# Performance work log

Measured on AMD Instinct MI355X. Metric: run time of the kernel, lower is better.

The kernel has to match this reference:

```python
import jax, jax.numpy as jnp
import numpy as np

EMBED_DIM = 1024
NUM_HEADS = 16
HEAD_DIM = EMBED_DIM // NUM_HEADS
B, N = 2, 2048
BIAS_S = 32


def _interp_matrix(n, s):
    # Bilinear interpolation (align_corners=True) along one axis as an (n, s) matrix.
    pos = jnp.arange(n, dtype=jnp.float32) * ((s - 1) / (n - 1))
    i0 = jnp.floor(pos).astype(jnp.int32)
    i1 = jnp.minimum(i0 + 1, s - 1)
    frac = pos - i0.astype(jnp.float32)
    rows = jnp.arange(n)
    M = jnp.zeros((n, s), dtype=jnp.float32)
    M = M.at[rows, i0].add(1.0 - frac).at[rows, i1].add(frac)
    return M


def setup_inputs() -> dict:
    key = jax.random.key(0)
    ks = jax.random.split(key, 12)
    std = 0.02
    d = {
        'x': jax.random.normal(ks[0], (B, N, EMBED_DIM), dtype=jnp.float32),
        'Wq': jax.random.normal(ks[1], (EMBED_DIM, EMBED_DIM), dtype=jnp.float32) * std,
        'bq': jnp.zeros((EMBED_DIM,), dtype=jnp.float32),
        'Wk': jax.random.normal(ks[2], (EMBED_DIM, EMBED_DIM), dtype=jnp.float32) * std,
        'bk': jnp.zeros((EMBED_DIM,), dtype=jnp.float32),
        'Wv': jax.random.normal(ks[3], (EMBED_DIM, EMBED_DIM), dtype=jnp.float32) * std,
        'bv': jnp.zeros((EMBED_DIM,), dtype=jnp.float32),
        'Wo': jax.random.normal(ks[4], (EMBED_DIM, EMBED_DIM), dtype=jnp.float32) * std,
        'bo': jnp.zeros((EMBED_DIM,), dtype=jnp.float32),
        'gamma': jnp.ones((EMBED_DIM,), dtype=jnp.float32),
        'beta': jnp.zeros((EMBED_DIM,), dtype=jnp.float32),
        'rel_bias': jax.random.normal(ks[5], (NUM_HEADS, BIAS_S, BIAS_S), dtype=jnp.float32) * std,
    }
    return d


def reference(x, Wq, bq, Wk, bk, Wv, bv, Wo, bo, gamma, beta, rel_bias):
    Bx, Nx, C = x.shape
    H, D = NUM_HEADS, HEAD_DIM
    scale = 1.0 / jnp.sqrt(jnp.float32(D))

    # LayerNorm
    mu = jnp.mean(x, axis=-1, keepdims=True)
    var = jnp.mean(jnp.square(x - mu), axis=-1, keepdims=True)
    xn = (x - mu) * jax.lax.rsqrt(var + 1e-5) * gamma + beta

    q = (xn @ Wq.T + bq).reshape(Bx, Nx, H, D).transpose(0, 2, 1, 3)
    k = (xn @ Wk.T + bk).reshape(Bx, Nx, H, D).transpose(0, 2, 1, 3)
    v = (xn @ Wv.T + bv).reshape(Bx, Nx, H, D).transpose(0, 2, 1, 3)

    attn = jnp.einsum('bhnd,bhmd->bhnm', q, k) * scale  # [B,H,N,N]

    # Bilinear interp of rel_pos_bias (H,32,32) -> (H,N,N), align_corners=True
    M = _interp_matrix(Nx, BIAS_S)  # (N, 32)
    rel = jnp.einsum('ni,hij,mj->hnm', M, rel_bias, M)
    rel = rel.at[:, -1, :].set(0.0).at[:, :, -1].set(0.0)
    attn = attn + rel[None]

    mask = jnp.triu(jnp.ones((Nx, Nx), dtype=bool), k=1)
    attn = jnp.where(mask, -jnp.inf, attn)
    attn = jax.nn.softmax(attn, axis=-1)

    out = jnp.einsum('bhnm,bhmd->bhnd', attn, v)
    out = out.transpose(0, 2, 1, 3).reshape(Bx, Nx, C)
    out = out @ Wo.T + bo  # dropout is identity in eval mode
    return out
```

## Files before the change

### kernel.cpp

```cpp
#include <hip/hip_runtime.h>
#include <hip/hip_bf16.h>

#define EMBED 1024
#define NHEADS 16
#define HDIM 64
#define NB 2
#define NSEQ 2048
#define NTOK (NB*NSEQ)

using short8  = __attribute__((ext_vector_type(8))) short;
using short4v = __attribute__((ext_vector_type(4))) short;
using f32x4   = __attribute__((ext_vector_type(4))) float;

#define INV_LN2 1.4426950408889634f

__device__ __forceinline__ short f2bf(float x) {
  __hip_bfloat16 h = __float2bfloat16(x);
  short s;
  __builtin_memcpy(&s, &h, 2);
  return s;
}

#define GLDS16(gp, lp) __builtin_amdgcn_global_load_lds( \
    (const __attribute__((address_space(1))) unsigned int*)(const void*)(gp), \
    (__attribute__((address_space(3))) unsigned int*)(void*)(lp), 16, 0, 0)

__global__ __launch_bounds__(256) void lncast_kernel(const float* __restrict__ x,
    const float* __restrict__ gamma, const float* __restrict__ beta, short* __restrict__ xn,
    const float* __restrict__ Wq, const float* __restrict__ Wk,
    const float* __restrict__ Wv, const float* __restrict__ Wo,
    short* __restrict__ wqb, short* __restrict__ wkb,
    short* __restrict__ wvb, short* __restrict__ wob) {
  const int bid = blockIdx.x;
  const int tid = threadIdx.x;
  if (bid < NTOK) {
    const float* xr = x + (size_t)bid * EMBED;
    float4 v = *(const float4*)(xr + tid * 4);
    float s  = v.x + v.y + v.z + v.w;
    float s2 = v.x*v.x + v.y*v.y + v.z*v.z + v.w*v.w;
#pragma unroll
    for (int off = 32; off; off >>= 1) {
      s  += __shfl_down(s, off);
      s2 += __shfl_down(s2, off);
    }
    __shared__ float red[8];
    const int wv = tid >> 6, ln = tid & 63;
    if (ln == 0) { red[wv] = s; red[4 + wv] = s2; }
    __syncthreads();
    s  = red[0] + red[1] + red[2] + red[3];
    s2 = red[4] + red[5] + red[6] + red[7];
    const float mu  = s * (1.0f / EMBED);
    const float var = s2 * (1.0f / EMBED) - mu * mu;
    const float inv = rsqrtf(var + 1e-5f);
    float4 g  = *(const float4*)(gamma + tid * 4);
    float4 bt = *(const float4*)(beta + tid * 4);
    short4v o;
    o[0] = f2bf((v.x - mu) * inv * g.x + bt.x);
    o[1] = f2bf((v.y - mu) * inv * g.y + bt.y);
    o[2] = f2bf((v.z - mu) * inv * g.z + bt.z);
    o[3] = f2bf((v.w - mu) * inv * g.w + bt.w);
    *(short4v*)(xn + (size_t)bid * EMBED + tid * 4) = o;
  } else {
    const int i = (bid - NTOK) * 1024 + tid * 4;
    const int wsel = i >> 20;
    const int off  = i & 1048575;
    const float* s = (wsel == 0) ? Wq : (wsel == 1) ? Wk : (wsel == 2) ? Wv : Wo;
    short* o       = (wsel == 0) ? wqb : (wsel == 1) ? wkb : (wsel == 2) ? wvb : wob;
    float4 v = *(const float4*)(s + off);
    short4v r;
    r[0] = f2bf(v.x); r[1] = f2bf(v.y); r[2] = f2bf(v.z); r[3] = f2bf(v.w);
    *(short4v*)(o + off) = r;
  }
}

__global__ __launch_bounds__(512, 4) void qkv2ph_kernel(
    const short* __restrict__ A, const short* __restrict__ Wcat,
    const float* __restrict__ b0, const float* __restrict__ b1, const float* __restrict__ b2,
    short* __restrict__ O0, short* __restrict__ O1, short* __restrict__ O2) {
  constexpr int K = 1024;
  const int orig = blockIdx.x;
  const int swzb = (orig & 7) * 64 + (orig >> 3);
  const int tn = swzb & 15, tm = swzb >> 4;

  const int tid = threadIdx.x;
  const int w = tid >> 6, lane = tid & 63;
  const int wr = w >> 2, wc = w & 3;
  const int g = lane >> 4, c = lane & 15;

  __shared__ short As[2][128 * 64];
  __shared__ short Bs[2][192 * 64];

  f32x4 acc[4][3];
#pragma unroll
  for (int i = 0; i < 4; i++)
#pragma unroll
    for (int j = 0; j < 3; j++) acc[i][j] = (f32x4){0.f, 0.f, 0.f, 0.f};

  const int sr  = tid >> 3;
  const int sc8 = (tid & 7) * 8;
  const int ssw = (sr & 7) << 3;
  const short* ga = A    + (size_t)(tm * 128) * K;
  const short* gb = Wcat + (size_t)(tn * 192) * K;

  auto STAGE = [&](int buf, int kt) {
#pragma unroll
    for (int u = 0; u < 2; u++) {
      const int row = u * 64 + sr;
      GLDS16(ga + (size_t)row * K + kt * 64 + (sc8 ^ ssw), &As[buf][row * 64 + sc8]);
    }
#pragma unroll
    for (int u = 0; u < 3; u++) {
      const int row = u * 64 + sr;
      GLDS16(gb + (size_t)row * K + kt * 64 + (sc8 ^ ssw), &Bs[buf][row * 64 + sc8]);
    }
  };

  STAGE(0, 0);
  __syncthreads();

  for (int kt = 0; kt < 16; ++kt) {
    const int cur = kt & 1;
    if (kt + 1 < 16) STAGE(cur ^ 1, kt + 1);
    const short* as = As[cur];
    const short* bs = Bs[cur];
#pragma unroll
    for (int ks = 0; ks < 2; ks++) {
      short8 af[4], bf[3];
#pragma unroll
      for (int mi = 0; mi < 4; mi++) {
        const int row = wr * 64 + mi * 16 + c;
        af[mi] = *(const short8*)&as[row * 64 + ((ks * 32 + g * 8) ^ ((row & 7) << 3))];
      }
#pragma unroll
      for (int ni = 0; ni < 3; ni++) {
        const int row = wc * 48 + ni * 16 + c;
        bf[ni] = *(const short8*)&bs[row * 64 + ((ks * 32 + g * 8) ^ ((row & 7) << 3))];
      }
      __builtin_amdgcn_s_setprio(1);
#pragma unroll
      for (int mi = 0; mi < 4; mi++)
#pragma unroll
        for (int ni = 0; ni < 3; ni++)
          acc[mi][ni] = __builtin_amdgcn_mfma_f32_16x16x32_bf16(af[mi], bf[ni], acc[mi][ni], 0, 0, 0);
      __builtin_amdgcn_s_setprio(0);
    }
    __syncthreads();
  }

#pragma unroll
  for (int ni = 0; ni < 3; ni++) {
    const int col = tn * 192 + wc * 48 + ni * 16 + c;
    const int sel = col >> 10, lc = col & 1023;
    short* O        = (sel == 0) ? O0 : (sel == 1) ? O1 : O2;
    const float* bb = (sel == 0) ? b0 : (sel == 1) ? b1 : b2;
    const float bsv = bb[lc];
#pragma unroll
    for (int mi = 0; mi < 4; mi++) {
      const int row = tm * 128 + wr * 64 + mi * 16 + g * 4;
#pragma unroll
      for (int j = 0; j < 4; j++)
        O[(size_t)(row + j) * 1024 + lc] = f2bf(acc[mi][ni][j] + bsv);
    }
  }
}

template<bool F32OUT>
__global__ __launch_bounds__(256) void gemm_kernel(
    const short* __restrict__ A, const short* __restrict__ Bw,
    const float* __restrict__ bias, void* __restrict__ Cout) {
  constexpr int K = 1024, NOUT = 1024;
  const int tn = blockIdx.x, tm = blockIdx.y;
  const int tid = threadIdx.x, w = tid >> 6, lane = tid & 63;
  const int wm = w >> 1, wn = w & 1;
  const int g = lane >> 4, c = lane & 15;

  __shared__ short As[128 * 32];
  __shared__ short Bs[128 * 32];

  f32x4 acc[4][4];
#pragma unroll
  for (int i = 0; i < 4; i++)
#pragma unroll
    for (int j = 0; j < 4; j++) acc[i][j] = (f32x4){0.f, 0.f, 0.f, 0.f};

  const int crow = tid >> 2;
  const int ckc  = tid & 3;
  const short* ga = A  + (size_t)(tm * 128 + crow) * K + ckc * 8;
  const short* gb = Bw + (size_t)(tn * 128 + crow) * K + ckc * 8;
  short* la = &As[tid * 8];
  short* lb = &Bs[tid * 8];

  for (int k0 = 0; k0 < K; k0 += 32) {
    __syncthreads();
    GLDS16(ga + k0, la);
    GLDS16(ga + k0 + (size_t)64 * K, la + 64 * 32);
    GLDS16(gb + k0, lb);
    GLDS16(gb + k0 + (size_t)64 * K, lb + 64 * 32);
    __syncthreads();
    short8 af[4], bfr[4];
#pragma unroll
    for (int mi = 0; mi < 4; mi++)
      af[mi] = *(const short8*)&As[(wm * 64 + mi * 16 + c) * 32 + g * 8];
#pragma unroll
    for (int ni = 0; ni < 4; ni++)
      bfr[ni] = *(const short8*)&Bs[(wn * 64 + ni * 16 + c) * 32 + g * 8];
#pragma unroll
    for (int mi = 0; mi < 4; mi++)
#pragma unroll
      for (int ni = 0; ni < 4; ni++)
        acc[mi][ni] = __builtin_amdgcn_mfma_f32_16x16x32_bf16(af[mi], bfr[ni], acc[mi][ni], 0, 0, 0);
  }

#pragma unroll
  for (int ni = 0; ni < 4; ni++) {
    const int col = tn * 128 + wn * 64 + ni * 16 + c;
    const float bs = bias[col];
#pragma unroll
    for (int mi = 0; mi < 4; mi++) {
#pragma unroll
      for (int j = 0; j < 4; j++) {
        const int row = tm * 128 + wm * 64 + mi * 16 + g * 4 + j;
        const float v = acc[mi][ni][j] + bs;
        if constexpr (F32OUT)
          ((float*)Cout)[(size_t)row * NOUT + col] = v;
        else
          ((short*)Cout)[(size_t)row * NOUT + col] = f2bf(v);
      }
    }
  }
}

__global__ __launch_bounds__(256) void vtrans_kernel(const short* __restrict__ vb,
                                                     short* __restrict__ vt) {
  const int n0 = blockIdx.x * 64;
  const int bh = blockIdx.y;
  const int b = bh >> 4, h = bh & 15;
  const int tid = threadIdx.x;
  __shared__ short tl[64 * 68];

  const int r  = tid >> 3;
  const int c8 = (tid & 7) * 8;
#pragma unroll
  for (int i = 0; i < 2; i++) {
    const int row = r + i * 32;
    short8 v = *(const short8*)(vb + (size_t)(b * NSEQ + n0 + row) * EMBED + h * 64 + c8);
    *(short8*)&tl[row * 68 + c8] = v;
  }
  __syncthreads();
  const int d  = tid >> 2;
  const int ns = (tid & 3) * 16;
  short8 o0, o1;
#pragma unroll
  for (int e = 0; e < 8; e++) {
    o0[e] = tl[(ns + e) * 68 + d];
    o1[e] = tl[(ns + 8 + e) * 68 + d];
  }
  short* dst = vt + ((size_t)((b * 16 + h) * 64 + d)) * 2048 + n0 + ns;
  *(short8*)dst = o0;
  *(short8*)(dst + 8) = o1;
}

__global__ __launch_bounds__(512, 4) void attn_kernel(
    const short* __restrict__ Qm, const short* __restrict__ Km, const short* __restrict__ Vt,
    const float* __restrict__ relb, short* __restrict__ ctx) {
  const int bid = blockIdx.x;
  const int bh  = bid & 31;
  const int idx = bid >> 5;
  const int qpair = (idx < 8) ? (15 - idx) : (idx - 8);
  const int b = bh >> 4, h = bh & 15;
  const int tid = threadIdx.x, w = tid >> 6, lane = tid & 63;
  const int g = lane >> 4, c = lane & 15;
  constexpr float S31 = 31.0f / 2047.0f;
  constexpr float CSC = 0.125f * INV_LN2;

  __shared__ short k_lds[2][64 * 64];
  __shared__ short vt_lds[2][64 * 64];
  __shared__ short p_lds[8][16 * 64];
  __shared__ short rbf[128 * 32];
  __shared__ short u_lds[2][64 * 40];

  const int qbase = qpair * 128;
  const size_t bhq = (size_t)b * NSEQ * EMBED + h * HDIM;
  const short* vtb = Vt + (size_t)((b << 4) + h) * 64 * 2048;

  short8 qf[2];
  {
    const short* qp = Qm + bhq + (size_t)(qbase + w * 16 + c) * EMBED;
    qf[0] = *(const short8*)(qp + g * 8);
    qf[1] = *(const short8*)(qp + 32 + g * 8);
  }

  const int srow = tid >> 3;
  const int sd0  = (tid & 7) * 8;
  const int swz  = (srow & 7) << 3;

  auto buildU = [&](int buf, int kv) {
    if (tid < 64) {
      short* ur = &u_lds[buf][tid * 40];
      *(int4*)&ur[0]  = (int4){0, 0, 0, 0};
      *(int4*)&ur[8]  = (int4){0, 0, 0, 0};
      *(int4*)&ur[16] = (int4){0, 0, 0, 0};
      *(int4*)&ur[24] = (int4){0, 0, 0, 0};
      const int m = kv + tid;
      if (m != NSEQ - 1) {
        const float pos = m * S31;
        const int i0 = (int)pos;
        const float fr = pos - (float)i0;
        ur[i0]     = f2bf(1.0f - fr);
        ur[i0 + 1] = f2bf(fr);
      }
    }
  };

  GLDS16(Km + bhq + (size_t)srow * EMBED + (sd0 ^ swz), &k_lds[0][srow * 64 + sd0]);
  GLDS16(vtb + (size_t)srow * 2048 + (sd0 ^ swz),       &vt_lds[0][srow * 64 + sd0]);
  for (int i = tid; i < 128 * 32; i += 512) {
    const int qr = i >> 5, jj = i & 31;
    const int qg0 = qbase + qr;
    float rv = 0.f;
    if (qg0 != NSEQ - 1) {
      const float pos = qg0 * S31;
      const int i0 = (int)pos;
      const int i1 = min(i0 + 1, 31);
      const float fr = pos - (float)i0;
      const float* T = relb + h * 1024;
      rv = ((1.f - fr) * T[i0 * 32 + jj] + fr * T[i1 * 32 + jj]) * 8.0f;
    }
    rbf[i] = f2bf(rv);
  }
  buildU(0, 0);
  __syncthreads();

  const short8 rq = *(const short8*)&rbf[(w * 16 + c) * 32 + g * 8];

  float mrow = -3.0e38f, lrow = 0.f;
  f32x4 oacc[4];
#pragma unroll
  for (int db = 0; db < 4; db++) oacc[db] = (f32x4){0.f, 0.f, 0.f, 0.f};

  const int qg  = qbase + w * 16 + c;
  const int qhi = qbase + w * 16 + 15;
  const int csw = (c & 7) << 3;
  const int nkv = 2 * qpair + 2;

  for (int kt = 0; kt < nkv; kt++) {
    const int cur = kt & 1;
    const int kv0 = kt * 64;

    if (kt + 1 < nkv) {
      GLDS16(Km + bhq + (size_t)(kv0 + 64 + srow) * EMBED + (sd0 ^ swz),
             &k_lds[cur ^ 1][srow * 64 + sd0]);
      GLDS16(vtb + (size_t)srow * 2048 + (kv0 + 64) + (sd0 ^ swz),
             &vt_lds[cur ^ 1][srow * 64 + sd0]);
      buildU(cur ^ 1, kv0 + 64);
    }

    if (kv0 <= qhi) {
      const short* kl = &k_lds[cur][0];
      const short* vl = &vt_lds[cur][0];
      const short* ul = &u_lds[cur][0];

      f32x4 st[4];
#pragma unroll
      for (int mb = 0; mb < 4; mb++) st[mb] = (f32x4){0.f, 0.f, 0.f, 0.f};
      __builtin_amdgcn_s_setprio(1);
#pragma unroll
      for (int kh = 0; kh < 2; kh++) {
        const int dk = kh * 32 + g * 8;
#pragma unroll
        for (int mb = 0; mb < 4; mb++) {
          const int row = mb * 16 + c;
          short8 kf = *(const short8*)&kl[row * 64 + (dk ^ ((row & 7) << 3))];
          st[mb] = __builtin_amdgcn_mfma_f32_16x16x32_bf16(kf, qf[kh], st[mb], 0, 0, 0);
        }
      }
#pragma unroll
      for (int mb = 0; mb < 4; mb++) {
        short8 uf = *(const short8*)&ul[(mb * 16 + c) * 40 + g * 8];
        st[mb] = __builtin_amdgcn_mfma_f32_16x16x32_bf16(uf, rq, st[mb], 0, 0, 0);
      }
      __builtin_amdgcn_s_setprio(0);

      const bool diag = (kv0 + 63 > qg);
      if (diag) {
#pragma unroll
        for (int mb = 0; mb < 4; mb++)
#pragma unroll
          for (int j = 0; j < 4; j++) {
            const int mg = kv0 + mb * 16 + g * 4 + j;
            if (mg > qg) st[mb][j] = -1.0e38f;
          }
      }
      float pmr = -3.0e38f;
#pragma unroll
      for (int mb = 0; mb < 4; mb++)
#pragma unroll
        for (int j = 0; j < 4; j++) pmr = fmaxf(pmr, st[mb][j]);
      float pmax = pmr * CSC;
      pmax = fmaxf(pmax, __shfl_xor(pmax, 16));
      pmax = fmaxf(pmax, __shfl_xor(pmax, 32));

      if (!__all(pmax - mrow <= 11.6f)) {
        const float mnew = fmaxf(mrow, pmax);
        const float al = exp2f(mrow - mnew);
        mrow = mnew;
        lrow *= al;
        float alj[4];
#pragma unroll
        for (int j = 0; j < 4; j++) alj[j] = __shfl(al, g * 4 + j);
#pragma unroll
        for (int db = 0; db < 4; db++)
#pragma unroll
          for (int j = 0; j < 4; j++) oacc[db][j] *= alj[j];
      }

      float p[4][4];
      float rs = 0.f;
#pragma unroll
      for (int mb = 0; mb < 4; mb++)
#pragma unroll
        for (int j = 0; j < 4; j++) {
          const float pe = exp2f(fmaf(st[mb][j], CSC, -mrow));
          p[mb][j] = pe;
          rs += pe;
        }
      rs += __shfl_xor(rs, 16);
      rs += __shfl_xor(rs, 32);
      lrow += rs;

      short* pw = &p_lds[w][0];
#pragma unroll
      for (int mb = 0; mb < 4; mb++)
#pragma unroll
        for (int jh = 0; jh < 2; jh++) {
          const int m = mb * 16 + g * 4 + jh * 2;
          unsigned int pk = ((unsigned int)(unsigned short)f2bf(p[mb][jh * 2 + 1]) << 16)
                          |  (unsigned int)(unsigned short)f2bf(p[mb][jh * 2]);
          *(unsigned int*)&pw[c * 64 + (m ^ csw)] = pk;
        }

      __builtin_amdgcn_s_setprio(1);
#pragma unroll
      for (int kb = 0; kb < 2; kb++) {
        const int m0 = kb * 32 + g * 8;
        short8 pa = *(const short8*)&pw[c * 64 + (m0 ^ csw)];
#pragma unroll
        for (int db = 0; db < 4; db++) {
          const int d = db * 16 + c;
          short8 vf = *(const short8*)&vl[d * 64 + (m0 ^ ((d & 7) << 3))];
          oacc[db] = __builtin_amdgcn_mfma_f32_16x16x32_bf16(pa, vf, oacc[db], 0, 0, 0);
        }
      }
      __builtin_amdgcn_s_setprio(0);
    }
    __syncthreads();
  }

  float linv[4];
#pragma unroll
  for (int j = 0; j < 4; j++) linv[j] = 1.f / __shfl(lrow, g * 4 + j);
#pragma unroll
  for (int j = 0; j < 4; j++) {
    short* op = ctx + bhq + (size_t)(qbase + w * 16 + g * 4 + j) * EMBED;
#pragma unroll
    for (int db = 0; db < 4; db++)
      op[db * 16 + c] = f2bf(oacc[db][j] * linv[j]);
  }
}

extern "C" void kernel_launch(void* const* d_in, const int* in_sizes, int n_in,
                              void* d_out, int out_size, void* d_ws, size_t ws_size,
                              hipStream_t stream) {
  const float* x     = (const float*)d_in[0];
  const float* Wq    = (const float*)d_in[1];
  const float* bq    = (const float*)d_in[2];
  const float* Wk    = (const float*)d_in[3];
  const float* bk    = (const float*)d_in[4];
  const float* Wv    = (const float*)d_in[5];
  const float* bv    = (const float*)d_in[6];
  const float* Wo    = (const float*)d_in[7];
  const float* bo    = (const float*)d_in[8];
  const float* gamma = (const float*)d_in[9];
  const float* beta  = (const float*)d_in[10];
  const float* relb  = (const float*)d_in[11];
  float* out = (float*)d_out;

  char* ws = (char*)d_ws;
  short* xn  = (short*)ws; ws += (size_t)NTOK * EMBED * 2;
  short* wqb = (short*)ws; ws += (size_t)EMBED * EMBED * 2;
  short* wkb = (short*)ws; ws += (size_t)EMBED * EMBED * 2;
  short* wvb = (short*)ws; ws += (size_t)EMBED * EMBED * 2;
  short* wob = (short*)ws; ws += (size_t)EMBED * EMBED * 2;
  short* qb  = (short*)ws; ws += (size_t)NTOK * EMBED * 2;
  short* kb_ = (short*)ws; ws += (size_t)NTOK * EMBED * 2;
  short* vb  = (short*)ws; ws += (size_t)NTOK * EMBED * 2;
  short* ctx = (short*)ws; ws += (size_t)NTOK * EMBED * 2;
  short* vtb = xn;

  lncast_kernel<<<dim3(NTOK + 4096), dim3(256), 0, stream>>>(
      x, gamma, beta, xn, Wq, Wk, Wv, Wo, wqb, wkb, wvb, wob);
  qkv2ph_kernel<<<dim3(512), dim3(512), 0, stream>>>(
      xn, wqb, bq, bk, bv, qb, kb_, vb);
  vtrans_kernel<<<dim3(32, 32), dim3(256), 0, stream>>>(vb, vtb);
  attn_kernel<<<dim3(512), dim3(512), 0, stream>>>(qb, kb_, vtb, relb, ctx);
  gemm_kernel<true><<<dim3(8, 32), dim3(256), 0, stream>>>(ctx, wob, bo, (void*)out);
}
```

Measured before the change: 211.5 us.

## Give each attention wave 32 query rows and double-buffer the output projection

The attention kernel drops from 512 to 256 threads, and each wave now handles two 16-row query groups. This lets every K and V fragment read from LDS feed two MFMAs, halving LDS traffic per flop, at the cost of more registers and fewer waves to hide latency. The output-projection GEMM is replaced by a double-buffered 128x64 tile kernel with K-step 64, swizzled LDS, block-index swizzling for cache locality and a launch grid of 512 blocks. The aim is better load/compute overlap and more blocks in flight.

```diff
diff --git a/kernel.cpp b/kernel.cpp
--- a/kernel.cpp
+++ b/kernel.cpp
@@ -164,68 +164,90 @@
   }
 }
 
-template<bool F32OUT>
-__global__ __launch_bounds__(256) void gemm_kernel(
+__global__ __launch_bounds__(256, 2) void proj2ph_kernel(
     const short* __restrict__ A, const short* __restrict__ Bw,
-    const float* __restrict__ bias, void* __restrict__ Cout) {
-  constexpr int K = 1024, NOUT = 1024;
-  const int tn = blockIdx.x, tm = blockIdx.y;
-  const int tid = threadIdx.x, w = tid >> 6, lane = tid & 63;
-  const int wm = w >> 1, wn = w & 1;
+    const float* __restrict__ bias, float* __restrict__ Cout) {
+  constexpr int K = 1024;
+  const int orig = blockIdx.x;
+  const int swzb = (orig & 7) * 64 + (orig >> 3);
+  const int tn = swzb & 15, tm = swzb >> 4;
+
+  const int tid = threadIdx.x;
+  const int w = tid >> 6, lane = tid & 63;
+  const int wr = w >> 1, wc = w & 1;
   const int g = lane >> 4, c = lane & 15;
 
-  __shared__ short As[128 * 32];
-  __shared__ short Bs[128 * 32];
-
-  f32x4 acc[4][4];
+  __shared__ short As[2][128 * 64];
+  __shared__ short Bs[2][64 * 64];
+
+  f32x4 acc[4][2];
 #pragma unroll
   for (int i = 0; i < 4; i++)
 #pragma unroll
-    for (int j = 0; j < 4; j++) acc[i][j] = (f32x4){0.f, 0.f, 0.f, 0.f};
-
-  const int crow = tid >> 2;
-  const int ckc  = tid & 3;
-  const short* ga = A  + (size_t)(tm * 128 + crow) * K + ckc * 8;
-  const short* gb = Bw + (size_t)(tn * 128 + crow) * K + ckc * 8;
-  short* la = &As[tid * 8];
-  short* lb = &Bs[tid * 8];
-
-  for (int k0 = 0; k0 < K; k0 += 32) {
+    for (int j = 0; j < 2; j++) acc[i][j] = (f32x4){0.f, 0.f, 0.f, 0.f};
+
+  const int sr8 = tid >> 3;
+  const int sd0 = (tid & 7) * 8;
+  const short* ga = A  + (size_t)(tm * 128) * K;
+  const short* gb = Bw + (size_t)(tn * 64) * K;
+
+  auto STAGE = [&](int buf, int kt) {
+#pragma unroll
+    for (int i = 0; i < 4; i++) {
+      const int row = i * 32 + sr8;
+      const int sw = (row & 7) << 3;
+      GLDS16(ga + (size_t)row * K + kt * 64 + (sd0 ^ sw), &As[buf][row * 64 + sd0]);
+    }
+#pragma unroll
+    for (int i = 0; i < 2; i++) {
+      const int row = i * 32 + sr8;
+      const int sw = (row & 7) << 3;
+      GLDS16(gb + (size_t)row * K + kt * 64 + (sd0 ^ sw), &Bs[buf][row * 64 + sd0]);
+    }
+  };
+
+  STAGE(0, 0);
+  __syncthreads();
+
+  for (int kt = 0; kt < 16; ++kt) {
+    const int cur = kt & 1;
+    if (kt + 1 < 16) STAGE(cur ^ 1, kt + 1);
+    const short* as = As[cur];
+    const short* bs = Bs[cur];
+#pragma unroll
+    for (int ks = 0; ks < 2; ks++) {
+      short8 af[4], bf[2];
+#pragma unroll
+      for (int mi = 0; mi < 4; mi++) {
+        const int row = wr * 64 + mi * 16 + c;
+        af[mi] = *(const short8*)&as[row * 64 + ((ks * 32 + g * 8) ^ ((row & 7) << 3))];
+      }
+#pragma unroll
+      for (int ni = 0; ni < 2; ni++) {
+        const int row = wc * 32 + ni * 16 + c;
+        bf[ni] = *(const short8*)&bs[row * 64 + ((ks * 32 + g * 8) ^ ((row & 7) << 3))];
+      }
+      __builtin_amdgcn_s_setprio(1);
+#pragma unroll
+      for (int mi = 0; mi < 4; mi++)
+#pragma unroll
+        for (int ni = 0; ni < 2; ni++)
+          acc[mi][ni] = __builtin_amdgcn_mfma_f32_16x16x32_bf16(af[mi], bf[ni], acc[mi][ni], 0, 0, 0);
+      __builtin_amdgcn_s_setprio(0);
+    }
     __syncthreads();
-    GLDS16(ga + k0, la);
-    GLDS16(ga + k0 + (size_t)64 * K, la + 64 * 32);
-    GLDS16(gb + k0, lb);
-    GLDS16(gb + k0 + (size_t)64 * K, lb + 64 * 32);
-    __syncthreads();
-    short8 af[4], bfr[4];
-#pragma unroll
-    for (int mi = 0; mi < 4; mi++)
-      af[mi] = *(const short8*)&As[(wm * 64 + mi * 16 + c) * 32 + g * 8];
-#pragma unroll
-    for (int ni = 0; ni < 4; ni++)
-      bfr[ni] = *(const short8*)&Bs[(wn * 64 + ni * 16 + c) * 32 + g * 8];
-#pragma unroll
-    for (int mi = 0; mi < 4; mi++)
-#pragma unroll
-      for (int ni = 0; ni < 4; ni++)
-        acc[mi][ni] = __builtin_amdgcn_mfma_f32_16x16x32_bf16(af[mi], bfr[ni], acc[mi][ni], 0, 0, 0);
-  }
-
-#pragma unroll
-  for (int ni = 0; ni < 4; ni++) {
-    const int col = tn * 128 + wn * 64 + ni * 16 + c;
-    const float bs = bias[col];
+  }
+
+#pragma unroll
+  for (int ni = 0; ni < 2; ni++) {
+    const int col = tn * 64 + wc * 32 + ni * 16 + c;
+    const float bsv = bias[col];
 #pragma unroll
     for (int mi = 0; mi < 4; mi++) {
-#pragma unroll
-      for (int j = 0; j < 4; j++) {
-        const int row = tm * 128 + wm * 64 + mi * 16 + g * 4 + j;
-        const float v = acc[mi][ni][j] + bs;
-        if constexpr (F32OUT)
-          ((float*)Cout)[(size_t)row * NOUT + col] = v;
-        else
-          ((short*)Cout)[(size_t)row * NOUT + col] = f2bf(v);
-      }
+      const int row = tm * 128 + wr * 64 + mi * 16 + g * 4;
+#pragma unroll
+      for (int j = 0; j < 4; j++)
+        Cout[(size_t)(row + j) * 1024 + col] = acc[mi][ni][j] + bsv;
     }
   }
 }
@@ -260,7 +282,7 @@
   *(short8*)(dst + 8) = o1;
 }
 
-__global__ __launch_bounds__(512, 4) void attn_kernel(
+__global__ __launch_bounds__(256, 2) void attn_kernel(
     const short* __restrict__ Qm, const short* __restrict__ Km, const short* __restrict__ Vt,
     const float* __restrict__ relb, short* __restrict__ ctx) {
   const int bid = blockIdx.x;
@@ -275,7 +297,7 @@
 
   __shared__ short k_lds[2][64 * 64];
   __shared__ short vt_lds[2][64 * 64];
-  __shared__ short p_lds[8][16 * 64];
+  __shared__ short p_lds[4][32 * 64];
   __shared__ short rbf[128 * 32];
   __shared__ short u_lds[2][64 * 40];
 
@@ -283,16 +305,16 @@
   const size_t bhq = (size_t)b * NSEQ * EMBED + h * HDIM;
   const short* vtb = Vt + (size_t)((b << 4) + h) * 64 * 2048;
 
-  short8 qf[2];
-  {
-    const short* qp = Qm + bhq + (size_t)(qbase + w * 16 + c) * EMBED;
-    qf[0] = *(const short8*)(qp + g * 8);
-    qf[1] = *(const short8*)(qp + 32 + g * 8);
-  }
-
-  const int srow = tid >> 3;
-  const int sd0  = (tid & 7) * 8;
-  const int swz  = (srow & 7) << 3;
+  short8 qf[2][2];
+#pragma unroll
+  for (int grp = 0; grp < 2; grp++) {
+    const short* qp = Qm + bhq + (size_t)(qbase + w * 32 + grp * 16 + c) * EMBED;
+    qf[grp][0] = *(const short8*)(qp + g * 8);
+    qf[grp][1] = *(const short8*)(qp + 32 + g * 8);
+  }
+
+  const int sr8 = tid >> 3;
+  const int sd0 = (tid & 7) * 8;
 
   auto buildU = [&](int buf, int kv) {
     if (tid < 64) {
@@ -312,9 +334,14 @@
     }
   };
 
-  GLDS16(Km + bhq + (size_t)srow * EMBED + (sd0 ^ swz), &k_lds[0][srow * 64 + sd0]);
-  GLDS16(vtb + (size_t)srow * 2048 + (sd0 ^ swz),       &vt_lds[0][srow * 64 + sd0]);
-  for (int i = tid; i < 128 * 32; i += 512) {
+#pragma unroll
+  for (int i = 0; i < 2; i++) {
+    const int row = i * 32 + sr8;
+    const int sw = (row & 7) << 3;
+    GLDS16(Km + bhq + (size_t)row * EMBED + (sd0 ^ sw), &k_lds[0][row * 64 + sd0]);
+    GLDS16(vtb + (size_t)row * 2048 + (sd0 ^ sw),       &vt_lds[0][row * 64 + sd0]);
+  }
+  for (int i = tid; i < 128 * 32; i += 256) {
     const int qr = i >> 5, jj = i & 31;
     const int qg0 = qbase + qr;
     float rv = 0.f;
@@ -331,15 +358,20 @@
   buildU(0, 0);
   __syncthreads();
 
-  const short8 rq = *(const short8*)&rbf[(w * 16 + c) * 32 + g * 8];
-
-  float mrow = -3.0e38f, lrow = 0.f;
-  f32x4 oacc[4];
-#pragma unroll
-  for (int db = 0; db < 4; db++) oacc[db] = (f32x4){0.f, 0.f, 0.f, 0.f};
-
-  const int qg  = qbase + w * 16 + c;
-  const int qhi = qbase + w * 16 + 15;
+  short8 rq[2];
+#pragma unroll
+  for (int grp = 0; grp < 2; grp++)
+    rq[grp] = *(const short8*)&rbf[(w * 32 + grp * 16 + c) * 32 + g * 8];
+
+  float mrow[2] = {-3.0e38f, -3.0e38f}, lrow[2] = {0.f, 0.f};
+  f32x4 oacc[2][4];
+#pragma unroll
+  for (int grp = 0; grp < 2; grp++)
+#pragma unroll
+    for (int db = 0; db < 4; db++) oacc[grp][db] = (f32x4){0.f, 0.f, 0.f, 0.f};
+
+  const int qgg[2] = {qbase + w * 32 + c, qbase + w * 32 + 16 + c};
+  const int qhi = qbase + w * 32 + 31;
   const int csw = (c & 7) << 3;
   const int nkv = 2 * qpair + 2;
 
@@ -348,10 +380,15 @@
     const int kv0 = kt * 64;
 
     if (kt + 1 < nkv) {
-      GLDS16(Km + bhq + (size_t)(kv0 + 64 + srow) * EMBED + (sd0 ^ swz),
-             &k_lds[cur ^ 1][srow * 64 + sd0]);
-      GLDS16(vtb + (size_t)srow * 2048 + (kv0 + 64) + (sd0 ^ swz),
-             &vt_lds[cur ^ 1][srow * 64 + sd0]);
+#pragma unroll
+      for (int i = 0; i < 2; i++) {
+        const int row = i * 32 + sr8;
+        const int sw = (row & 7) << 3;
+        GLDS16(Km + bhq + (size_t)(kv0 + 64 + row) * EMBED + (sd0 ^ sw),
+               &k_lds[cur ^ 1][row * 64 + sd0]);
+        GLDS16(vtb + (size_t)row * 2048 + (kv0 + 64) + (sd0 ^ sw),
+               &vt_lds[cur ^ 1][row * 64 + sd0]);
+      }
       buildU(cur ^ 1, kv0 + 64);
     }
 
@@ -360,9 +397,12 @@
       const short* vl = &vt_lds[cur][0];
       const short* ul = &u_lds[cur][0];
 
-      f32x4 st[4];
-#pragma unroll
-      for (int mb = 0; mb < 4; mb++) st[mb] = (f32x4){0.f, 0.f, 0.f, 0.f};
+      f32x4 st[2][4];
+#pragma unroll
+      for (int grp = 0; grp < 2; grp++)
+#pragma unroll
+        for (int mb = 0; mb < 4; mb++) st[grp][mb] = (f32x4){0.f, 0.f, 0.f, 0.f};
+
       __builtin_amdgcn_s_setprio(1);
 #pragma unroll
       for (int kh = 0; kh < 2; kh++) {
@@ -371,84 +411,101 @@
         for (int mb = 0; mb < 4; mb++) {
           const int row = mb * 16 + c;
           short8 kf = *(const short8*)&kl[row * 64 + (dk ^ ((row & 7) << 3))];
-          st[mb] = __builtin_amdgcn_mfma_f32_16x16x32_bf16(kf, qf[kh], st[mb], 0, 0, 0);
+          st[0][mb] = __builtin_amdgcn_mfma_f32_16x16x32_bf16(kf, qf[0][kh], st[0][mb], 0, 0, 0);
+          st[1][mb] = __builtin_amdgcn_mfma_f32_16x16x32_bf16(kf, qf[1][kh], st[1][mb], 0, 0, 0);
         }
       }
 #pragma unroll
       for (int mb = 0; mb < 4; mb++) {
         short8 uf = *(const short8*)&ul[(mb * 16 + c) * 40 + g * 8];
-        st[mb] = __builtin_amdgcn_mfma_f32_16x16x32_bf16(uf, rq, st[mb], 0, 0, 0);
+        st[0][mb] = __builtin_amdgcn_mfma_f32_16x16x32_bf16(uf, rq[0], st[0][mb], 0, 0, 0);
+        st[1][mb] = __builtin_amdgcn_mfma_f32_16x16x32_bf16(uf, rq[1], st[1][mb], 0, 0, 0);
       }
       __builtin_amdgcn_s_setprio(0);
 
-      const bool diag = (kv0 + 63 > qg);
-      if (diag) {
+      float pmax[2];
+#pragma unroll
+      for (int grp = 0; grp < 2; grp++) {
+        const int qg = qgg[grp];
+        if (kv0 + 63 > qg) {
+#pragma unroll
+          for (int mb = 0; mb < 4; mb++)
+#pragma unroll
+            for (int j = 0; j < 4; j++) {
+              const int mg = kv0 + mb * 16 + g * 4 + j;
+              if (mg > qg) st[grp][mb][j] = -1.0e38f;
+            }
+        }
+        float pmr = -3.0e38f;
 #pragma unroll
         for (int mb = 0; mb < 4; mb++)
 #pragma unroll
+          for (int j = 0; j < 4; j++) pmr = fmaxf(pmr, st[grp][mb][j]);
+        float pm = pmr * CSC;
+        pm = fmaxf(pm, __shfl_xor(pm, 16));
+        pm = fmaxf(pm, __shfl_xor(pm, 32));
+        pmax[grp] = pm;
+      }
+
+      if (!__all((pmax[0] - mrow[0] <= 11.6f) && (pmax[1] - mrow[1] <= 11.6f))) {
+#pragma unroll
+        for (int grp = 0; grp < 2; grp++) {
+          const float mnew = fmaxf(mrow[grp], pmax[grp]);
+          const float al = exp2f(mrow[grp] - mnew);
+          mrow[grp] = mnew;
+          lrow[grp] *= al;
+          float alj[4];
+#pragma unroll
+          for (int j = 0; j < 4; j++) alj[j] = __shfl(al, g * 4 + j);
+#pragma unroll
+          for (int db = 0; db < 4; db++)
+#pragma unroll
+            for (int j = 0; j < 4; j++) oacc[grp][db][j] *= alj[j];
+        }
+      }
+
+      float p[2][4][4];
+#pragma unroll
+      for (int grp = 0; grp < 2; grp++) {
+        float rs = 0.f;
+#pragma unroll
+        for (int mb = 0; mb < 4; mb++)
+#pragma unroll
           for (int j = 0; j < 4; j++) {
-            const int mg = kv0 + mb * 16 + g * 4 + j;
-            if (mg > qg) st[mb][j] = -1.0e38f;
+            const float pe = exp2f(fmaf(st[grp][mb][j], CSC, -mrow[grp]));
+            p[grp][mb][j] = pe;
+            rs += pe;
           }
-      }
-      float pmr = -3.0e38f;
-#pragma unroll
-      for (int mb = 0; mb < 4; mb++)
-#pragma unroll
-        for (int j = 0; j < 4; j++) pmr = fmaxf(pmr, st[mb][j]);
-      float pmax = pmr * CSC;
-      pmax = fmaxf(pmax, __shfl_xor(pmax, 16));
-      pmax = fmaxf(pmax, __shfl_xor(pmax, 32));
-
-      if (!__all(pmax - mrow <= 11.6f)) {
-        const float mnew = fmaxf(mrow, pmax);
-        const float al = exp2f(mrow - mnew);
-        mrow = mnew;
-        lrow *= al;
-        float alj[4];
-#pragma unroll
-        for (int j = 0; j < 4; j++) alj[j] = __shfl(al, g * 4 + j);
-#pragma unroll
-        for (int db = 0; db < 4; db++)
-#pragma unroll
-          for (int j = 0; j < 4; j++) oacc[db][j] *= alj[j];
-      }
-
-      float p[4][4];
-      float rs = 0.f;
-#pragma unroll
-      for (int mb = 0; mb < 4; mb++)
-#pragma unroll
-        for (int j = 0; j < 4; j++) {
-          const float pe = exp2f(fmaf(st[mb][j], CSC, -mrow));
-          p[mb][j] = pe;
-          rs += pe;
-        }
-      rs += __shfl_xor(rs, 16);
-      rs += __shfl_xor(rs, 32);
-      lrow += rs;
+        rs += __shfl_xor(rs, 16);
+        rs += __shfl_xor(rs, 32);
+        lrow[grp] += rs;
+      }
 
       short* pw = &p_lds[w][0];
 #pragma unroll
-      for (int mb = 0; mb < 4; mb++)
-#pragma unroll
-        for (int jh = 0; jh < 2; jh++) {
-          const int m = mb * 16 + g * 4 + jh * 2;
-          unsigned int pk = ((unsigned int)(unsigned short)f2bf(p[mb][jh * 2 + 1]) << 16)
-                          |  (unsigned int)(unsigned short)f2bf(p[mb][jh * 2]);
-          *(unsigned int*)&pw[c * 64 + (m ^ csw)] = pk;
-        }
+      for (int grp = 0; grp < 2; grp++)
+#pragma unroll
+        for (int mb = 0; mb < 4; mb++)
+#pragma unroll
+          for (int jh = 0; jh < 2; jh++) {
+            const int m = mb * 16 + g * 4 + jh * 2;
+            unsigned int pk = ((unsigned int)(unsigned short)f2bf(p[grp][mb][jh * 2 + 1]) << 16)
+                            |  (unsigned int)(unsigned short)f2bf(p[grp][mb][jh * 2]);
+            *(unsigned int*)&pw[(grp * 16 + c) * 64 + (m ^ csw)] = pk;
+          }
 
       __builtin_amdgcn_s_setprio(1);
 #pragma unroll
       for (int kb = 0; kb < 2; kb++) {
         const int m0 = kb * 32 + g * 8;
-        short8 pa = *(const short8*)&pw[c * 64 + (m0 ^ csw)];
+        short8 pa0 = *(const short8*)&pw[c * 64 + (m0 ^ csw)];
+        short8 pa1 = *(const short8*)&pw[(16 + c) * 64 + (m0 ^ csw)];
 #pragma unroll
         for (int db = 0; db < 4; db++) {
           const int d = db * 16 + c;
           short8 vf = *(const short8*)&vl[d * 64 + (m0 ^ ((d & 7) << 3))];
-          oacc[db] = __builtin_amdgcn_mfma_f32_16x16x32_bf16(pa, vf, oacc[db], 0, 0, 0);
+          oacc[0][db] = __builtin_amdgcn_mfma_f32_16x16x32_bf16(pa0, vf, oacc[0][db], 0, 0, 0);
+          oacc[1][db] = __builtin_amdgcn_mfma_f32_16x16x32_bf16(pa1, vf, oacc[1][db], 0, 0, 0);
         }
       }
       __builtin_amdgcn_s_setprio(0);
@@ -456,16 +513,16 @@
     __syncthreads();
   }
 
-  float linv[4];
-#pragma unroll
-  for (int j = 0; j < 4; j++) linv[j] = 1.f / __shfl(lrow, g * 4 + j);
-#pragma unroll
-  for (int j = 0; j < 4; j++) {
-    short* op = ctx + bhq + (size_t)(qbase + w * 16 + g * 4 + j) * EMBED;
-#pragma unroll
-    for (int db = 0; db < 4; db++)
-      op[db * 16 + c] = f2bf(oacc[db][j] * linv[j]);
-  }
+#pragma unroll
+  for (int grp = 0; grp < 2; grp++)
+#pragma unroll
+    for (int j = 0; j < 4; j++) {
+      const float linv = 1.f / __shfl(lrow[grp], g * 4 + j);
+      short* op = ctx + bhq + (size_t)(qbase + w * 32 + grp * 16 + g * 4 + j) * EMBED;
+#pragma unroll
+      for (int db = 0; db < 4; db++)
+        op[db * 16 + c] = f2bf(oacc[grp][db][j] * linv);
+    }
 }
 
 extern "C" void kernel_launch(void* const* d_in, const int* in_sizes, int n_in,
@@ -502,6 +559,6 @@
   qkv2ph_kernel<<<dim3(512), dim3(512), 0, stream>>>(
       xn, wqb, bq, bk, bv, qb, kb_, vb);
   vtrans_kernel<<<dim3(32, 32), dim3(256), 0, stream>>>(vb, vtb);
-  attn_kernel<<<dim3(512), dim3(512), 0, stream>>>(qb, kb_, vtb, relb, ctx);
-  gemm_kernel<true><<<dim3(8, 32), dim3(256), 0, stream>>>(ctx, wob, bo, (void*)out);
-}
+  attn_kernel<<<dim3(512), dim3(256), 0, stream>>>(qb, kb_, vtb, relb, ctx);
+  proj2ph_kernel<<<dim3(512), dim3(256), 0, stream>>>(ctx, wob, bo, out);
+}
```

Result: no change. 208.8 us (-1.2%).
